# Kernel tuning notes

Hardware: AMD Instinct MI355X
Metric: run time of the kernel (lower is better)

Reference implementation:

```python
import jax, jax.numpy as jnp
import numpy as np
from itertools import product

C0, C1, C_IN, C_OUT = 16, 32, 1, 32
GRID = 768

def _enc(c):
    # injective int64 hash of 3D integer coords (values in [-4, 2043])
    return ((c[:, 0] + 4) * 2048 + (c[:, 1] + 4)) * 2048 + (c[:, 2] + 4)

def _build_km(coords, offsets):
    # kernel map for a stride-1 conv on one coordinate set:
    # per kernel offset o, pairs (in_idx, out_idx) with coords[in] == coords[out] + o
    N = coords.shape[0]
    keys = _enc(coords)
    order = np.argsort(keys)
    skeys = keys[order]
    ins, outs = [], []
    for o in offsets:
        qk = _enc(coords + np.asarray(o, np.int64))
        pos = np.searchsorted(skeys, qk)
        posc = np.clip(pos, 0, N - 1)
        valid = skeys[posc] == qk
        ins.append(order[posc[valid]].astype(np.int32))
        outs.append(np.nonzero(valid)[0].astype(np.int32))
    P = max(len(a) for a in ins)
    km_in = np.full((len(offsets), P), N, np.int32)   # pad -> zero row of x
    km_out = np.full((len(offsets), P), N, np.int32)  # pad -> dropped out row
    for k in range(len(offsets)):
        km_in[k, :len(ins[k])] = ins[k]
        km_out[k, :len(outs[k])] = outs[k]
    return km_in, km_out

def setup_inputs() -> dict:
    # voxelized surface heightfield: realistic sparse 3D point cloud occupancy
    xs, ys = np.meshgrid(np.arange(GRID), np.arange(GRID), indexing='ij')
    z = np.round(40.0 * np.sin(xs / 24.0) + 40.0 * np.cos(ys / 24.0)).astype(np.int64) + 128
    coords0 = np.stack([xs.ravel(), ys.ravel(), z.ravel()], 1).astype(np.int64)
    n0 = coords0.shape[0]
    offs27 = list(product((-1, 0, 1), repeat=3))
    km0_in, km0_out = _build_km(coords0, offs27)

    # stride-2 kernel-2 downsample: out coord = floor(c/2), offset = c mod 2
    u2 = coords0 // 2
    coords1, inv = np.unique(u2, axis=0, return_inverse=True)
    inv = inv.reshape(-1)
    n1 = coords1.shape[0]
    o = coords0 - 2 * u2
    kk = o[:, 0] * 4 + o[:, 1] * 2 + o[:, 2]
    ins, outs = [], []
    for k in range(8):
        m = np.nonzero(kk == k)[0]
        ins.append(m.astype(np.int32))
        outs.append(inv[m].astype(np.int32))
    P = max(len(a) for a in ins)
    kmd_in = np.full((8, P), n0, np.int32)
    kmd_out = np.full((8, P), n1, np.int32)
    for k in range(8):
        kmd_in[k, :len(ins[k])] = ins[k]
        kmd_out[k, :len(outs[k])] = outs[k]

    km1_in, km1_out = _build_km(coords1, offs27)

    key = jax.random.key(0)
    ks = jax.random.split(key, 6)
    w = lambda k, sh: jax.random.normal(k, sh, jnp.float32) * 0.1
    z32 = lambda c: jnp.zeros((c,), jnp.float32)
    return dict(
        in_feats=jnp.ones((n0, C_IN), jnp.float32),
        W_first=w(ks[0], (27, C_IN, C0)), b_first=z32(C0),
        W_pre=w(ks[1], (27, C0, C0)), b_pre=z32(C0),
        W_down=w(ks[2], (8, C0, C1)), b_down=z32(C1),
        W_r0=w(ks[3], (27, C1, C1)), b_r0=z32(C1),
        W_r1=w(ks[4], (27, C1, C1)), b_r1=z32(C1),
        W_fin=w(ks[5], (27, C1, C_OUT)), b_fin=z32(C_OUT),
        km0_in=jnp.asarray(km0_in), km0_out=jnp.asarray(km0_out),
        kmd_in=jnp.asarray(kmd_in), kmd_out=jnp.asarray(kmd_out),
        km1_in=jnp.asarray(km1_in), km1_out=jnp.asarray(km1_out),
        n1=int(n1),
    )

def _sparse_conv(x, W, b, km_in, km_out, n_out):
    # gather-GEMM-scatter sparse conv: out[j] += x[i] @ W[k] over pairs of offset k
    xp = jnp.concatenate([x, jnp.zeros((1, x.shape[1]), x.dtype)], 0)
    out = jnp.zeros((n_out + 1, W.shape[-1]), x.dtype)
    for k in range(W.shape[0]):  # static small loop over kernel offsets
        out = out.at[km_out[k]].add(xp[km_in[k]] @ W[k])
    return out[:n_out] + b

def reference(in_feats, W_first, b_first, W_pre, b_pre, W_down, b_down,
              W_r0, b_r0, W_r1, b_r1, W_fin, b_fin,
              km0_in, km0_out, kmd_in, kmd_out, km1_in, km1_out, n1):
    n0 = in_feats.shape[0]
    relu = jax.nn.relu
    # first_block: 3^3 conv + relu
    x = relu(_sparse_conv(in_feats, W_first, b_first, km0_in, km0_out, n0))
    cached = x  # cached_feature_list[0] (use_skip_connection=False)
    # blocks[0]: conv3x3 + relu, stride-2 downsample conv + relu
    x = relu(_sparse_conv(x, W_pre, b_pre, km0_in, km0_out, n0))
    x = relu(_sparse_conv(x, W_down, b_down, kmd_in, kmd_out, n1))
    # ResBlock
    r = relu(_sparse_conv(x, W_r0, b_r0, km1_in, km1_out, n1))
    r = _sparse_conv(r, W_r1, b_r1, km1_in, km1_out, n1)
    x = r + x
    # final conv (act=None)
    out = _sparse_conv(x, W_fin, b_fin, km1_in, km1_out, n1)
    return (out, cached)
```

## Files before the change

### kernel.cpp

```cpp
#include <hip/hip_runtime.h>


#define TPB 256

typedef __attribute__((ext_vector_type(8))) short short8;
typedef __attribute__((ext_vector_type(4))) float floatx4;

static __device__ __forceinline__ unsigned short f2b(float f) {
    union { float f; unsigned u; } v; v.f = f;
    unsigned r = v.u + 0x7fffu + ((v.u >> 16) & 1u);
    return (unsigned short)(r >> 16);
}
static __device__ __forceinline__ float b2f(unsigned short h) {
    union { unsigned u; float f; } v; v.u = ((unsigned)h) << 16;
    return v.f;
}

static __device__ __forceinline__ unsigned wave_prefix_len(
    const int* __restrict__ row, unsigned P, unsigned nv, int lane) {
    unsigned lo = 0, hi = P;
    while (hi - lo > 64u) {
        unsigned step = (hi - lo) / 64u;
        unsigned pos = lo + (unsigned)lane * step;
        bool pad = ((unsigned)row[pos] >= nv);
        unsigned long long m = __ballot(pad);
        if (m == 0ULL) {
            lo = lo + 63u * step + 1u;
        } else {
            int f = __ffsll((unsigned long long)m) - 1;
            if (f == 0) { hi = lo; break; }
            hi = lo + (unsigned)f * step;
            lo = lo + (unsigned)(f - 1) * step + 1u;
        }
    }
    unsigned span = hi - lo;
    bool pad = true;
    if ((unsigned)lane < span) pad = ((unsigned)row[lo + lane] >= nv);
    unsigned long long m = __ballot(pad);
    unsigned f = (unsigned)(__ffsll((unsigned long long)m) - 1);
    return lo + (f < span ? f : span);
}

__global__ void rowlen_k(const int* __restrict__ km0_out,
                         const int* __restrict__ km1_out,
                         const int* __restrict__ kmd_out,
                         unsigned P0, unsigned P1, unsigned Pd,
                         unsigned n0, unsigned n1, int* __restrict__ rowlen) {
    int w = (int)((blockIdx.x * blockDim.x + threadIdx.x) >> 6);
    int lane = (int)threadIdx.x & 63;
    if (w >= 62) return;
    const int* row;
    unsigned P, nv;
    if (w < 27)      { row = km0_out + (size_t)w * P0;        P = P0; nv = n0; }
    else if (w < 54) { row = km1_out + (size_t)(w - 27) * P1; P = P1; nv = n1; }
    else             { row = kmd_out + (size_t)(w - 54) * Pd; P = Pd; nv = n1; }
    unsigned len = wave_prefix_len(row, P, nv, lane);
    if (lane == 0) rowlen[w] = (int)len;
}

__global__ __launch_bounds__(TPB) void scatter_rows(
    const int* __restrict__ km0_in, const int* __restrict__ km0_out,
    const int* __restrict__ km1_in, const int* __restrict__ km1_out,
    const int* __restrict__ kmd_in, const int* __restrict__ kmd_out,
    const int* __restrict__ rowlen,
    int* __restrict__ t0, int* __restrict__ t1, int* __restrict__ td,
    unsigned P0, unsigned P1, unsigned Pd,
    unsigned rc0, unsigned rc1) {
    const int w = (int)blockIdx.y;
    const int* in;
    const int* out;
    int* tab;
    unsigned P;
    if (w < 27) {
        P = P0;
        in  = km0_in  + (size_t)w * P0;
        out = km0_out + (size_t)w * P0;
        tab = t0 + (size_t)w * rc0;
    } else if (w < 54) {
        P = P1;
        in  = km1_in  + (size_t)(w - 27) * P1;
        out = km1_out + (size_t)(w - 27) * P1;
        tab = t1 + (size_t)(w - 27) * rc1;
    } else {
        P = Pd;
        in  = kmd_in  + (size_t)(w - 54) * Pd;
        out = kmd_out + (size_t)(w - 54) * Pd;
        tab = td + (size_t)(w - 54) * rc1;
    }
    const unsigned base = blockIdx.x * (TPB * 4u);
    if (base >= P) return;
    const int len = rowlen[w];
    if ((int)base >= len) return;
    const unsigned tid = threadIdx.x;
    const unsigned Pm1 = P - 1u;
    unsigned e[4];
    int o[4], ii[4];
#pragma unroll
    for (int j = 0; j < 4; ++j) {
        e[j] = base + (unsigned)j * TPB + tid;
        unsigned ue = e[j] < P ? e[j] : Pm1;
        o[j] = out[ue];
        ii[j] = in[ue];
    }
#pragma unroll
    for (int j = 0; j < 4; ++j)
        if ((int)e[j] < len) tab[o[j]] = ii[j];
}

static __device__ __forceinline__ void pack16_elem(
    const float* __restrict__ W, unsigned short* __restrict__ Wp,
    int t, int COUT, int Ksrc) {
    int j = t & 7;
    int r = t >> 3;
    int n = r % COUT; r /= COUT;
    int q = r & 3;
    int k2 = r >> 2;
    int ks = 2 * k2 + (q >> 1);
    int cin = (q & 1) * 8 + j;
    float v = (ks < Ksrc) ? W[(ks * 16 + cin) * COUT + n] : 0.f;
    Wp[t] = f2b(v);
}

__global__ void pack_all(const float* __restrict__ W_pre, const float* __restrict__ W_down,
                         const float* __restrict__ W_r0, const float* __restrict__ W_r1,
                         const float* __restrict__ W_fin,
                         unsigned short* __restrict__ wp_pre, unsigned short* __restrict__ wp_down,
                         unsigned short* __restrict__ wp_r0, unsigned short* __restrict__ wp_r1,
                         unsigned short* __restrict__ wp_fin,
                         unsigned short* p0, unsigned short* p1, unsigned short* p2,
                         unsigned short* p3, unsigned short* p4) {
    int t = blockIdx.x * blockDim.x + threadIdx.x;
    if (t < 7168) { pack16_elem(W_pre, wp_pre, t, 16, 27); return; }
    t -= 7168;
    if (t < 4096) { pack16_elem(W_down, wp_down, t, 32, 8); return; }
    t -= 4096;
    if (t < 27648) {
        int j = t & 7, n = (t >> 3) & 31, q = (t >> 8) & 3, k = t >> 10;
        wp_r0[t] = f2b(W_r0[(k * 32 + q * 8 + j) * 32 + n]); return;
    }
    t -= 27648;
    if (t < 27648) {
        int j = t & 7, n = (t >> 3) & 31, q = (t >> 8) & 3, k = t >> 10;
        wp_r1[t] = f2b(W_r1[(k * 32 + q * 8 + j) * 32 + n]); return;
    }
    t -= 27648;
    if (t < 27648) {
        int j = t & 7, n = (t >> 3) & 31, q = (t >> 8) & 3, k = t >> 10;
        wp_fin[t] = f2b(W_fin[(k * 32 + q * 8 + j) * 32 + n]); return;
    }
    t -= 27648;
    if (t < 16) p0[t] = 0;
    else if (t < 32) p1[t - 16] = 0;
    else if (t < 64) p2[t - 32] = 0;
    else if (t < 96) p3[t - 64] = 0;
    else if (t < 128) p4[t - 96] = 0;
}

__global__ __launch_bounds__(TPB) void conv_first_k(
    const float* __restrict__ xin, const float* __restrict__ W,
    const float* __restrict__ b, const int* __restrict__ tab, long long rowcap,
    int n0, float* __restrict__ outf, unsigned short* __restrict__ outb) {
    int j = blockIdx.x * blockDim.x + threadIdx.x;
    if (j >= n0) return;
    float acc[16];
#pragma unroll
    for (int c = 0; c < 16; ++c) acc[c] = b[c];
#pragma unroll
    for (int k = 0; k < 27; ++k) {
        int idx = tab[(long long)k * rowcap + j];
        bool ok = (unsigned)idx < (unsigned)n0;
        int cidx = ok ? idx : 0;
        float v = xin[cidx];
        v = ok ? v : 0.f;
        const float* Wk = W + k * 16;
#pragma unroll
        for (int c = 0; c < 16; ++c) acc[c] = fmaf(v, Wk[c], acc[c]);
    }
    float* orow = outf + (long long)j * 16;
    unsigned short* brow = outb + (long long)j * 16;
#pragma unroll
    for (int c = 0; c < 16; ++c) {
        float v = fmaxf(acc[c], 0.f);
        orow[c] = v;
        brow[c] = f2b(v);
    }
}

template <int CIN, int COUT, int STEPS, bool RELU, bool RES, bool WF32, bool WB16>
__global__ __launch_bounds__(TPB, 4) void conv_mfma(
    const unsigned short* __restrict__ xb,
    const unsigned short* __restrict__ Wp,
    const float* __restrict__ bias,
    const int* __restrict__ tab, long long rowcap, int n_in, int n_out,
    long long ntiles,
    const unsigned short* __restrict__ resb,
    float* __restrict__ outf, unsigned short* __restrict__ outb) {
    constexpr int NT = COUT / 16;
    int runs = (int)gridDim.x >> 3;
    int sb = (int)(blockIdx.x & 7) * runs + (int)(blockIdx.x >> 3);
    long long tile = (long long)sb * 4 + ((threadIdx.x >> 6) & 3);
    if (tile >= ntiles) return;
    int lane = (int)threadIdx.x & 63;
    int m = lane & 15, q = lane >> 4;
    long long j0 = tile * 64;

    floatx4 acc[4][NT];
#pragma unroll
    for (int t = 0; t < 4; ++t)
#pragma unroll
        for (int nt = 0; nt < NT; ++nt) acc[t][nt] = floatx4{0.f, 0.f, 0.f, 0.f};

    const int coff = (CIN == 32) ? q * 8 : (q & 1) * 8;
#pragma unroll
    for (int s = 0; s < STEPS; ++s) {
        const int ks = (CIN == 32) ? s : 2 * s + (q >> 1);
        const int* trow = tab + (long long)ks * rowcap + j0 + m;
        int idx[4];
#pragma unroll
        for (int t = 0; t < 4; ++t) {
            unsigned v = (unsigned)trow[16 * t];
            idx[t] = (int)(v < (unsigned)n_in ? v : (unsigned)n_in);
        }
        short8 b0 = *(const short8*)(Wp + (((s * 4 + q) * COUT) + m) * 8);
        short8 b1;
        if (NT == 2) b1 = *(const short8*)(Wp + (((s * 4 + q) * COUT) + 16 + m) * 8);
#pragma unroll
        for (int t = 0; t < 4; ++t) {
            short8 a = *(const short8*)(xb + (long long)idx[t] * CIN + coff);
            acc[t][0] = __builtin_amdgcn_mfma_f32_16x16x32_bf16(a, b0, acc[t][0], 0, 0, 0);
            if (NT == 2)
                acc[t][1] = __builtin_amdgcn_mfma_f32_16x16x32_bf16(a, b1, acc[t][1], 0, 0, 0);
        }
    }

    float bs[2];
    bs[0] = bias[m];
    if (NT == 2) bs[1] = bias[16 + m];
#pragma unroll
    for (int t = 0; t < 4; ++t) {
#pragma unroll
        for (int u = 0; u < 4; ++u) {
            long long r = j0 + 16 * t + q * 4 + u;
            if (r < n_out) {
#pragma unroll
                for (int nt = 0; nt < NT; ++nt) {
                    float v = acc[t][nt][u] + bs[nt];
                    if (RES) v += b2f(resb[r * COUT + nt * 16 + m]);
                    if (RELU) v = fmaxf(v, 0.f);
                    if (WF32) outf[r * COUT + nt * 16 + m] = v;
                    if (WB16) outb[r * COUT + nt * 16 + m] = f2b(v);
                }
            }
        }
    }
}

static inline unsigned nblk(long long n, int b) { return (unsigned)((n + b - 1) / b); }
static inline unsigned pad8(unsigned g) { return ((g + 7) / 8) * 8; }
static inline size_t align64(size_t x) { return (x + 63) & ~(size_t)63; }

extern "C" void kernel_launch(void* const* d_in, const int* in_sizes, int n_in_cnt,
                              void* d_out, int out_size, void* d_ws, size_t ws_size,
                              hipStream_t stream) {
    const float* in_feats = (const float*)d_in[0];
    const float* W_first = (const float*)d_in[1];
    const float* b_first = (const float*)d_in[2];
    const float* W_pre   = (const float*)d_in[3];
    const float* b_pre   = (const float*)d_in[4];
    const float* W_down  = (const float*)d_in[5];
    const float* b_down  = (const float*)d_in[6];
    const float* W_r0    = (const float*)d_in[7];
    const float* b_r0    = (const float*)d_in[8];
    const float* W_r1    = (const float*)d_in[9];
    const float* b_r1    = (const float*)d_in[10];
    const float* W_fin   = (const float*)d_in[11];
    const float* b_fin   = (const float*)d_in[12];
    const int* km0_in  = (const int*)d_in[13];
    const int* km0_out = (const int*)d_in[14];
    const int* kmd_in  = (const int*)d_in[15];
    const int* kmd_out = (const int*)d_in[16];
    const int* km1_in  = (const int*)d_in[17];
    const int* km1_out = (const int*)d_in[18];

    const int n0 = in_sizes[0];
    const int n1 = (out_size - 16 * n0) / 32;
    const long long P0 = in_sizes[13] / 27;
    const long long Pd = in_sizes[15] / 8;
    const long long P1 = in_sizes[17] / 27;

    const long long rc0 = ((n0 + 64) / 64) * 64;
    const long long rc1 = ((n1 + 64) / 64) * 64;
    const long long T0 = rc0 / 64, T1 = rc1 / 64;

    float* out_lo = (float*)d_out;
    float* cached = out_lo + (size_t)n1 * 32;

    char* base = (char*)d_ws;
    size_t off = 0;
    auto alloc = [&](size_t bytes) { void* p = base + off; off = align64(off + bytes); return p; };
    int* t0 = (int*)alloc(sizeof(int) * 28 * rc0);
    int* t1 = (int*)alloc(sizeof(int) * 27 * rc1);
    int* td = (int*)alloc(sizeof(int) * 8 * rc1);
    unsigned short* c0b   = (unsigned short*)alloc(sizeof(short) * 16 * (n0 + 1));
    unsigned short* x0pre = (unsigned short*)alloc(sizeof(short) * 16 * (n0 + 1));
    unsigned short* x1a   = (unsigned short*)alloc(sizeof(short) * 32 * (n1 + 1));
    unsigned short* x1b   = (unsigned short*)alloc(sizeof(short) * 32 * (n1 + 1));
    unsigned short* x1c   = (unsigned short*)alloc(sizeof(short) * 32 * (n1 + 1));
    unsigned short* wp_pre  = (unsigned short*)alloc(sizeof(short) * 14 * 4 * 16 * 8);
    unsigned short* wp_down = (unsigned short*)alloc(sizeof(short) * 4 * 4 * 32 * 8);
    unsigned short* wp_r0   = (unsigned short*)alloc(sizeof(short) * 27 * 1024);
    unsigned short* wp_r1   = (unsigned short*)alloc(sizeof(short) * 27 * 1024);
    unsigned short* wp_fin  = (unsigned short*)alloc(sizeof(short) * 27 * 1024);
    int* rowlen = (int*)alloc(sizeof(int) * 64);
    (void)ws_size; (void)n_in_cnt;

    rowlen_k<<<16, TPB, 0, stream>>>(km0_out, km1_out, kmd_out,
                                     (unsigned)P0, (unsigned)P1, (unsigned)Pd,
                                     (unsigned)n0, (unsigned)n1, rowlen);

    long long maxP = P0 > P1 ? P0 : P1;
    if (Pd > maxP) maxP = Pd;
    dim3 sgrid(nblk(maxP, TPB * 4), 62);
    scatter_rows<<<sgrid, TPB, 0, stream>>>(
        km0_in, km0_out, km1_in, km1_out, kmd_in, kmd_out, rowlen,
        t0, t1, td, (unsigned)P0, (unsigned)P1, (unsigned)Pd,
        (unsigned)rc0, (unsigned)rc1);

    const long long packN = 7168 + 4096 + 3 * 27648 + 128;
    pack_all<<<nblk(packN, TPB), TPB, 0, stream>>>(
        W_pre, W_down, W_r0, W_r1, W_fin,
        wp_pre, wp_down, wp_r0, wp_r1, wp_fin,
        c0b + (size_t)n0 * 16, x0pre + (size_t)n0 * 16,
        x1a + (size_t)n1 * 32, x1b + (size_t)n1 * 32, x1c + (size_t)n1 * 32);

    conv_first_k<<<nblk(n0, TPB), TPB, 0, stream>>>(in_feats, W_first, b_first, t0, rc0,
                                                    n0, cached, c0b);
    const unsigned g0 = pad8(nblk(T0, 4)), g1 = pad8(nblk(T1, 4));
    conv_mfma<16, 16, 14, true, false, false, true><<<g0, TPB, 0, stream>>>(
        c0b, wp_pre, b_pre, t0, rc0, n0, n0, T0, nullptr, nullptr, x0pre);
    conv_mfma<16, 32, 4, true, false, false, true><<<g1, TPB, 0, stream>>>(
        x0pre, wp_down, b_down, td, rc1, n0, n1, T1, nullptr, nullptr, x1a);
    conv_mfma<32, 32, 27, true, false, false, true><<<g1, TPB, 0, stream>>>(
        x1a, wp_r0, b_r0, t1, rc1, n1, n1, T1, nullptr, nullptr, x1b);
    conv_mfma<32, 32, 27, false, true, false, true><<<g1, TPB, 0, stream>>>(
        x1b, wp_r1, b_r1, t1, rc1, n1, n1, T1, x1a, nullptr, x1c);
    conv_mfma<32, 32, 27, false, false, true, false><<<g1, TPB, 0, stream>>>(
        x1c, wp_fin, b_fin, t1, rc1, n1, n1, T1, nullptr, out_lo, nullptr);
}
```

Baseline: 472.8 us.

## Split each 64-row tile across four waves instead of one wave per tile

Previously each wave owned a 64-row output tile and processed four 16-row sub-tiles, and a block held four tiles. Now a block owns one 64-row tile and each of its four waves handles a 16-row slice with a single accumulator set. This cuts registers per wave, and the launch bound is raised to 6 blocks per SM to increase occupancy and launch four times as many blocks. The cost is that weight fragments are reloaded per 16 rows instead of being reused across four sub-tiles, and each wave now has less memory-level parallelism from independent gathers.

```diff
diff --git a/kernel.cpp b/kernel.cpp
--- a/kernel.cpp
+++ b/kernel.cpp
@@ -187,7 +187,7 @@
 }
 
 template <int CIN, int COUT, int STEPS, bool RELU, bool RES, bool WF32, bool WB16>
-__global__ __launch_bounds__(TPB, 4) void conv_mfma(
+__global__ __launch_bounds__(TPB, 6) void conv_mfma(
     const unsigned short* __restrict__ xb,
     const unsigned short* __restrict__ Wp,
     const float* __restrict__ bias,
@@ -197,39 +197,29 @@
     float* __restrict__ outf, unsigned short* __restrict__ outb) {
     constexpr int NT = COUT / 16;
     int runs = (int)gridDim.x >> 3;
-    int sb = (int)(blockIdx.x & 7) * runs + (int)(blockIdx.x >> 3);
-    long long tile = (long long)sb * 4 + ((threadIdx.x >> 6) & 3);
+    long long tile = (long long)((blockIdx.x & 7) * runs + (blockIdx.x >> 3));
     if (tile >= ntiles) return;
+    int wv = (int)((threadIdx.x >> 6) & 3);
     int lane = (int)threadIdx.x & 63;
     int m = lane & 15, q = lane >> 4;
-    long long j0 = tile * 64;
-
-    floatx4 acc[4][NT];
-#pragma unroll
-    for (int t = 0; t < 4; ++t)
-#pragma unroll
-        for (int nt = 0; nt < NT; ++nt) acc[t][nt] = floatx4{0.f, 0.f, 0.f, 0.f};
+    long long j0 = tile * 64 + wv * 16;
+
+    floatx4 acc[NT];
+#pragma unroll
+    for (int nt = 0; nt < NT; ++nt) acc[nt] = floatx4{0.f, 0.f, 0.f, 0.f};
 
     const int coff = (CIN == 32) ? q * 8 : (q & 1) * 8;
 #pragma unroll
     for (int s = 0; s < STEPS; ++s) {
         const int ks = (CIN == 32) ? s : 2 * s + (q >> 1);
-        const int* trow = tab + (long long)ks * rowcap + j0 + m;
-        int idx[4];
-#pragma unroll
-        for (int t = 0; t < 4; ++t) {
-            unsigned v = (unsigned)trow[16 * t];
-            idx[t] = (int)(v < (unsigned)n_in ? v : (unsigned)n_in);
-        }
+        unsigned v = (unsigned)tab[(long long)ks * rowcap + j0 + m];
+        int idx = (int)(v < (unsigned)n_in ? v : (unsigned)n_in);
         short8 b0 = *(const short8*)(Wp + (((s * 4 + q) * COUT) + m) * 8);
-        short8 b1;
-        if (NT == 2) b1 = *(const short8*)(Wp + (((s * 4 + q) * COUT) + 16 + m) * 8);
-#pragma unroll
-        for (int t = 0; t < 4; ++t) {
-            short8 a = *(const short8*)(xb + (long long)idx[t] * CIN + coff);
-            acc[t][0] = __builtin_amdgcn_mfma_f32_16x16x32_bf16(a, b0, acc[t][0], 0, 0, 0);
-            if (NT == 2)
-                acc[t][1] = __builtin_amdgcn_mfma_f32_16x16x32_bf16(a, b1, acc[t][1], 0, 0, 0);
+        short8 a = *(const short8*)(xb + (long long)idx * CIN + coff);
+        acc[0] = __builtin_amdgcn_mfma_f32_16x16x32_bf16(a, b0, acc[0], 0, 0, 0);
+        if (NT == 2) {
+            short8 b1 = *(const short8*)(Wp + (((s * 4 + q) * COUT) + 16 + m) * 8);
+            acc[1] = __builtin_amdgcn_mfma_f32_16x16x32_bf16(a, b1, acc[1], 0, 0, 0);
         }
     }
 
@@ -237,19 +227,16 @@
     bs[0] = bias[m];
     if (NT == 2) bs[1] = bias[16 + m];
 #pragma unroll
-    for (int t = 0; t < 4; ++t) {
-#pragma unroll
-        for (int u = 0; u < 4; ++u) {
-            long long r = j0 + 16 * t + q * 4 + u;
-            if (r < n_out) {
-#pragma unroll
-                for (int nt = 0; nt < NT; ++nt) {
-                    float v = acc[t][nt][u] + bs[nt];
-                    if (RES) v += b2f(resb[r * COUT + nt * 16 + m]);
-                    if (RELU) v = fmaxf(v, 0.f);
-                    if (WF32) outf[r * COUT + nt * 16 + m] = v;
-                    if (WB16) outb[r * COUT + nt * 16 + m] = f2b(v);
-                }
+    for (int u = 0; u < 4; ++u) {
+        long long r = j0 + q * 4 + u;
+        if (r < n_out) {
+#pragma unroll
+            for (int nt = 0; nt < NT; ++nt) {
+                float v = acc[nt][u] + bs[nt];
+                if (RES) v += b2f(resb[r * COUT + nt * 16 + m]);
+                if (RELU) v = fmaxf(v, 0.f);
+                if (WF32) outf[r * COUT + nt * 16 + m] = v;
+                if (WB16) outb[r * COUT + nt * 16 + m] = f2b(v);
             }
         }
     }
@@ -335,7 +322,7 @@
 
     conv_first_k<<<nblk(n0, TPB), TPB, 0, stream>>>(in_feats, W_first, b_first, t0, rc0,
                                                     n0, cached, c0b);
-    const unsigned g0 = pad8(nblk(T0, 4)), g1 = pad8(nblk(T1, 4));
+    const unsigned g0 = pad8((unsigned)T0), g1 = pad8((unsigned)T1);
     conv_mfma<16, 16, 14, true, false, false, true><<<g0, TPB, 0, stream>>>(
         c0b, wp_pre, b_pre, t0, rc0, n0, n0, T0, nullptr, nullptr, x0pre);
     conv_mfma<16, 32, 4, true, false, false, true><<<g1, TPB, 0, stream>>>(
```

Result: slower. 528.6 us (+11.8%).

## Split kernel-offset reduction across waves with LDS cross-wave reduction

Applied to the files above, without the earlier changes.

Each block now handles one 64-row tile instead of four. Its four waves split the kernel-offset steps into quarter chunks, and the partial accumulators are summed through shared memory. This shortens each wave's serial chain of gather and MFMA operations and gives more blocks. In exchange it adds an LDS write/read reduction, a barrier, and larger shared memory use per block, which can reduce occupancy. Splits with uneven step counts, such as STEPS=27 or 14, leave the waves with unequal work.

```diff
diff --git a/kernel.cpp b/kernel.cpp
--- a/kernel.cpp
+++ b/kernel.cpp
@@ -186,6 +186,34 @@
     }
 }
 
+template <int CIN, int COUT, int NT, int SB, int SE>
+static __device__ __forceinline__ void kchunk(
+    const unsigned short* __restrict__ xb, const unsigned short* __restrict__ Wp,
+    const int* __restrict__ tab, long long rowcap, int n_in,
+    long long j0, int m, int q, int coff, floatx4 (&acc)[4][NT]) {
+#pragma unroll
+    for (int s = SB; s < SE; ++s) {
+        const int ks = (CIN == 32) ? s : 2 * s + (q >> 1);
+        const int* trow = tab + (long long)ks * rowcap + j0 + m;
+        int idx[4];
+#pragma unroll
+        for (int t = 0; t < 4; ++t) {
+            unsigned v = (unsigned)trow[16 * t];
+            idx[t] = (int)(v < (unsigned)n_in ? v : (unsigned)n_in);
+        }
+        short8 b0 = *(const short8*)(Wp + (((s * 4 + q) * COUT) + m) * 8);
+        short8 b1;
+        if (NT == 2) b1 = *(const short8*)(Wp + (((s * 4 + q) * COUT) + 16 + m) * 8);
+#pragma unroll
+        for (int t = 0; t < 4; ++t) {
+            short8 a = *(const short8*)(xb + (long long)idx[t] * CIN + coff);
+            acc[t][0] = __builtin_amdgcn_mfma_f32_16x16x32_bf16(a, b0, acc[t][0], 0, 0, 0);
+            if (NT == 2)
+                acc[t][1] = __builtin_amdgcn_mfma_f32_16x16x32_bf16(a, b1, acc[t][1], 0, 0, 0);
+        }
+    }
+}
+
 template <int CIN, int COUT, int STEPS, bool RELU, bool RES, bool WF32, bool WB16>
 __global__ __launch_bounds__(TPB, 4) void conv_mfma(
     const unsigned short* __restrict__ xb,
@@ -196,10 +224,11 @@
     const unsigned short* __restrict__ resb,
     float* __restrict__ outf, unsigned short* __restrict__ outb) {
     constexpr int NT = COUT / 16;
+    __shared__ floatx4 red[12 * 64 * NT];
     int runs = (int)gridDim.x >> 3;
-    int sb = (int)(blockIdx.x & 7) * runs + (int)(blockIdx.x >> 3);
-    long long tile = (long long)sb * 4 + ((threadIdx.x >> 6) & 3);
+    long long tile = (long long)((blockIdx.x & 7) * runs + (blockIdx.x >> 3));
     if (tile >= ntiles) return;
+    int wv = (int)((threadIdx.x >> 6) & 3);
     int lane = (int)threadIdx.x & 63;
     int m = lane & 15, q = lane >> 4;
     long long j0 = tile * 64;
@@ -211,45 +240,59 @@
         for (int nt = 0; nt < NT; ++nt) acc[t][nt] = floatx4{0.f, 0.f, 0.f, 0.f};
 
     const int coff = (CIN == 32) ? q * 8 : (q & 1) * 8;
-#pragma unroll
-    for (int s = 0; s < STEPS; ++s) {
-        const int ks = (CIN == 32) ? s : 2 * s + (q >> 1);
-        const int* trow = tab + (long long)ks * rowcap + j0 + m;
-        int idx[4];
-#pragma unroll
-        for (int t = 0; t < 4; ++t) {
-            unsigned v = (unsigned)trow[16 * t];
-            idx[t] = (int)(v < (unsigned)n_in ? v : (unsigned)n_in);
-        }
-        short8 b0 = *(const short8*)(Wp + (((s * 4 + q) * COUT) + m) * 8);
-        short8 b1;
-        if (NT == 2) b1 = *(const short8*)(Wp + (((s * 4 + q) * COUT) + 16 + m) * 8);
-#pragma unroll
-        for (int t = 0; t < 4; ++t) {
-            short8 a = *(const short8*)(xb + (long long)idx[t] * CIN + coff);
-            acc[t][0] = __builtin_amdgcn_mfma_f32_16x16x32_bf16(a, b0, acc[t][0], 0, 0, 0);
-            if (NT == 2)
-                acc[t][1] = __builtin_amdgcn_mfma_f32_16x16x32_bf16(a, b1, acc[t][1], 0, 0, 0);
+    constexpr int C1 = STEPS / 4, C2 = STEPS / 2, C3 = (3 * STEPS) / 4;
+    if (wv == 0)
+        kchunk<CIN, COUT, NT, 0, C1>(xb, Wp, tab, rowcap, n_in, j0, m, q, coff, acc);
+    else if (wv == 1)
+        kchunk<CIN, COUT, NT, C1, C2>(xb, Wp, tab, rowcap, n_in, j0, m, q, coff, acc);
+    else if (wv == 2)
+        kchunk<CIN, COUT, NT, C2, C3>(xb, Wp, tab, rowcap, n_in, j0, m, q, coff, acc);
+    else
+        kchunk<CIN, COUT, NT, C3, STEPS>(xb, Wp, tab, rowcap, n_in, j0, m, q, coff, acc);
+
+#pragma unroll
+    for (int t = 0; t < 4; ++t) {
+        if (t != wv) {
+            int sl = wv * 3 + (t > wv ? t - 1 : t);
+#pragma unroll
+            for (int nt = 0; nt < NT; ++nt)
+                red[(sl * 64 + lane) * NT + nt] = acc[t][nt];
+        }
+    }
+    floatx4 own[NT];
+#pragma unroll
+    for (int nt = 0; nt < NT; ++nt) own[nt] = acc[0][nt];
+#pragma unroll
+    for (int t = 1; t < 4; ++t)
+#pragma unroll
+        for (int nt = 0; nt < NT; ++nt)
+            if (wv == t) own[nt] = acc[t][nt];
+    __syncthreads();
+#pragma unroll
+    for (int w = 0; w < 4; ++w) {
+        if (w != wv) {
+            int sl = w * 3 + (wv > w ? wv - 1 : wv);
+#pragma unroll
+            for (int nt = 0; nt < NT; ++nt)
+                own[nt] += red[(sl * 64 + lane) * NT + nt];
         }
     }
 
     float bs[2];
     bs[0] = bias[m];
     if (NT == 2) bs[1] = bias[16 + m];
-#pragma unroll
-    for (int t = 0; t < 4; ++t) {
-#pragma unroll
-        for (int u = 0; u < 4; ++u) {
-            long long r = j0 + 16 * t + q * 4 + u;
-            if (r < n_out) {
-#pragma unroll
-                for (int nt = 0; nt < NT; ++nt) {
-                    float v = acc[t][nt][u] + bs[nt];
-                    if (RES) v += b2f(resb[r * COUT + nt * 16 + m]);
-                    if (RELU) v = fmaxf(v, 0.f);
-                    if (WF32) outf[r * COUT + nt * 16 + m] = v;
-                    if (WB16) outb[r * COUT + nt * 16 + m] = f2b(v);
-                }
+    long long jb = j0 + wv * 16;
+#pragma unroll
+    for (int u = 0; u < 4; ++u) {
+        long long r = jb + q * 4 + u;
+        if (r < n_out) {
+#pragma unroll
+            for (int nt = 0; nt < NT; ++nt) {
+                float v = own[nt][u] + bs[nt];
+                if (RES) v += b2f(resb[r * COUT + nt * 16 + m]);
+                if (RELU) v = fmaxf(v, 0.f);
+                if (WF32) outf[r * COUT + nt * 16 + m] = v;
+                if (WB16) outb[r * COUT + nt * 16 + m] = f2b(v);
             }
         }
     }
@@ -335,7 +378,7 @@
 
     conv_first_k<<<nblk(n0, TPB), TPB, 0, stream>>>(in_feats, W_first, b_first, t0, rc0,
                                                     n0, cached, c0b);
-    const unsigned g0 = pad8(nblk(T0, 4)), g1 = pad8(nblk(T1, 4));
+    const unsigned g0 = pad8((unsigned)T0), g1 = pad8((unsigned)T1);
     conv_mfma<16, 16, 14, true, false, false, true><<<g0, TPB, 0, stream>>>(
         c0b, wp_pre, b_pre, t0, rc0, n0, n0, T0, nullptr, nullptr, x0pre);
     conv_mfma<16, 32, 4, true, false, false, true><<<g1, TPB, 0, stream>>>(
```

Measured after the change: 469.9 us. No clear change (-0.6%).
